# Optimization experiments

Measured on AMD Instinct MI355X. Metric: run time of the kernel, lower is better.

The kernel has to match this reference:

```python
import jax, jax.numpy as jnp
import numpy as np

jax.config.update("jax_enable_x64", True)

MAX_LEN = 2048
D_MODEL = 2048
CONTEXT = 1
FUDGE = 0.01
MIN_PERIOD = 1
MAX_PERIOD = 1024
FORGOTTEN_AT = 0.01


def _init_params():
    # Mirrors LaplaceAggregation.__init__ with init_method='linspace', modify_real=True
    limit = np.log(np.finfo(np.float64).max) / MAX_LEN - FUDGE
    soft_high = np.log(FORGOTTEN_AT) / MAX_PERIOD
    soft_low = np.log(FORGOTTEN_AT) / MIN_PERIOD
    a_low = max(-limit + FUDGE, soft_low)
    a_high = max(min(-1e-6, soft_high), a_low)
    a = np.linspace(a_low, a_high, D_MODEL).reshape(1, 1, D_MODEL, CONTEXT)
    b = (2.0 * np.pi / np.linspace(MIN_PERIOD, MAX_PERIOD, D_MODEL)).reshape(1, 1, D_MODEL, CONTEXT)
    return jnp.asarray(a, jnp.float64), jnp.asarray(b, jnp.float64)


def setup_inputs() -> dict:
    key = jax.random.key(0)
    k1, k2, k3 = jax.random.split(key, 3)
    B, T, F = 8, 1024, D_MODEL
    x = jax.random.normal(k1, (B, T, F), dtype=jnp.float32)
    mem_real = jax.random.normal(k2, (B, 1, F, CONTEXT), dtype=jnp.float32)
    mem_imag = jax.random.normal(k3, (B, 1, F, CONTEXT), dtype=jnp.float32)
    a, b = _init_params()
    return {"x": x, "mem_real": mem_real, "mem_imag": mem_imag, "a": a, "b": b}


def reference(x, mem_real, mem_imag, a, b):
    # batched_recurrent_update path (1 < T < max_len)
    T = x.shape[1]
    f64, c128 = jnp.float64, jnp.complex128
    ab = a.astype(f64) + 1j * b.astype(f64)           # [1,1,F,C] complex

    def psi(t):  # t: [T] -> [1,T,F,C]
        return jnp.exp(ab * t.reshape(1, -1, 1, 1))

    # inner_idx[:T] = [max_len-1, ..., max_len-T]; outer_idx = -inner_idx
    inner = jnp.arange(MAX_LEN - 1, MAX_LEN - 1 - T, -1, dtype=f64)
    offset = jnp.arange(1, T + 1, dtype=f64)          # state_offset[:T]

    xc = x.astype(f64)[..., None].astype(c128)        # [B,T,F,1]
    z = jnp.cumsum(psi(inner) * xc, axis=1)           # [B,T,F,C]
    mem0 = (mem_real.astype(f64) + 1j * mem_imag.astype(f64))  # [B,1,F,C]
    out = psi(-inner) * z + mem0 * psi(offset)        # [B,T,F,C]
    return out.astype(jnp.complex64)
```

## Files before the change

kernel.cpp:

```cpp
#include <hip/hip_runtime.h>
#include <math.h>

#define BB 8
#define TT 1024
#define FF 2048
#define F4 (FF / 4)
#define F2H (FF / 2)
#define LCH 16
#define NCH 64
#define THR 512


typedef float vf4 __attribute__((ext_vector_type(4)));

__device__ __align__(16) float g_S[(size_t)BB * NCH * FF * 2];
__device__ __align__(16) float g_seed[(size_t)BB * NCH * FF * 2];
__device__ __align__(16) float g_lam[FF * 2];

__device__ inline bool ab_is_f64(const void* bp) {
    double bd = ((const double*)bp)[0];
    return (bd > 6.0 && bd < 6.6);
}

__device__ inline void load_ab4(const void* ap, const void* bp, int f,
                                double* av, double* bv) {
    if (ab_is_f64(bp)) {
#pragma unroll
        for (int k = 0; k < 4; ++k) {
            av[k] = ((const double*)ap)[f + k];
            bv[k] = ((const double*)bp)[f + k];
        }
    } else {
#pragma unroll
        for (int k = 0; k < 4; ++k) {
            av[k] = (double)((const float*)ap)[f + k];
            bv[k] = (double)((const float*)bp)[f + k];
        }
    }
}

__global__ void __launch_bounds__(THR)
k_reduce(const float4* __restrict__ x4, const void* __restrict__ a,
         const void* __restrict__ b) {
    int tid = threadIdx.x;
    int c   = blockIdx.x & (NCH - 1);
    int bb  = blockIdx.x >> 6;

    const float4* xp = x4 + (size_t)(bb * TT + c * LCH) * F4 + tid;
    float4 xv[LCH];
#pragma unroll
    for (int j = 0; j < LCH; ++j) xv[j] = xp[(size_t)j * F4];

    double av[4], bv[4];
    load_ab4(a, b, 4 * tid, av, bv);
    float lr[4], li[4];
#pragma unroll
    for (int k = 0; k < 4; ++k) {
        double m = exp(av[k]);
        double s, cth;
        sincos(bv[k], &s, &cth);
        lr[k] = (float)(m * cth);
        li[k] = (float)(m * s);
    }
    if (blockIdx.x == 0) {
        vf4 t0, t1;
        t0.x = lr[0]; t0.y = li[0]; t0.z = lr[1]; t0.w = li[1];
        t1.x = lr[2]; t1.y = li[2]; t1.z = lr[3]; t1.w = li[3];
        *(vf4*)&g_lam[8 * tid]     = t0;
        *(vf4*)&g_lam[8 * tid + 4] = t1;
    }

    float zr[4] = {0.f, 0.f, 0.f, 0.f}, zi[4] = {0.f, 0.f, 0.f, 0.f};
#pragma unroll
    for (int j = 0; j < LCH; ++j) {
        float xj[4] = {xv[j].x, xv[j].y, xv[j].z, xv[j].w};
#pragma unroll
        for (int k = 0; k < 4; ++k) {
            float nr = fmaf(lr[k], zr[k], fmaf(-li[k], zi[k], xj[k]));
            float ni = fmaf(lr[k], zi[k], li[k] * zr[k]);
            zr[k] = nr; zi[k] = ni;
        }
    }
    float* sp = &g_S[((size_t)(bb * NCH + c) * FF + 4 * tid) * 2];
    vf4 s0, s1;
    s0.x = zr[0]; s0.y = zi[0]; s0.z = zr[1]; s0.w = zi[1];
    s1.x = zr[2]; s1.y = zi[2]; s1.z = zr[3]; s1.w = zi[3];
    *(vf4*)sp       = s0;
    *(vf4*)(sp + 4) = s1;
}

__global__ void __launch_bounds__(THR)
k_scan(const float* __restrict__ mr, const float* __restrict__ mi,
       const void* __restrict__ a, const void* __restrict__ b) {
    int gid = blockIdx.x * THR + threadIdx.x;
    int f   = gid & (FF - 1);
    int bb  = gid >> 11;

    double av, bvv;
    if (ab_is_f64(b)) {
        av  = ((const double*)a)[f];
        bvv = ((const double*)b)[f];
    } else {
        av  = (double)((const float*)a)[f];
        bvv = (double)((const float*)b)[f];
    }
    double mm = exp((double)LCH * av), ms, mc;
    sincos((double)LCH * bvv, &ms, &mc);
    double m_r = mm * mc, m_i = mm * ms;
    double m0r = (double)mr[(size_t)bb * FF + f];
    double m0i = (double)mi[(size_t)bb * FF + f];

    double e_r = 1.0, e_i = 0.0;
    double P_r = 0.0, P_i = 0.0;
    for (int cc = 0; cc < NCH; ++cc) {
        size_t idx = ((size_t)(bb * NCH + cc) * FF + f) * 2;
        g_seed[idx]     = (float)(e_r * m0r - e_i * m0i + P_r);
        g_seed[idx + 1] = (float)(e_r * m0i + e_i * m0r + P_i);
        double Sr = (double)g_S[idx], Si = (double)g_S[idx + 1];
        double npr = m_r * P_r - m_i * P_i + Sr;
        double npi = m_r * P_i + m_i * P_r + Si;
        P_r = npr; P_i = npi;
        double ner = e_r * m_r - e_i * m_i;
        double nei = e_r * m_i + e_i * m_r;
        e_r = ner; e_i = nei;
    }
}

__global__ void __launch_bounds__(THR)
k_final(const float4* __restrict__ x4, float2* __restrict__ out2, size_t limit2) {
    int tid = threadIdx.x;
    int c   = blockIdx.x & (NCH - 1);
    int bb  = blockIdx.x >> 6;

    const float4* xp = x4 + (size_t)(bb * TT + c * LCH) * F4 + tid;
    float4 xv[LCH];
#pragma unroll
    for (int j = 0; j < LCH; ++j) xv[j] = xp[(size_t)j * F4];

    const float4* lp = (const float4*)&g_lam[8 * tid];
    float4 lA = lp[0], lB = lp[1];
    float lr[4] = {lA.x, lA.z, lB.x, lB.z};
    float li[4] = {lA.y, lA.w, lB.y, lB.w};
    const float4* sp =
        (const float4*)&g_seed[((size_t)(bb * NCH + c) * FF + 4 * tid) * 2];
    float4 s0 = sp[0], s1 = sp[1];
    float wr[4] = {s0.x, s0.z, s1.x, s1.z};
    float wi[4] = {s0.y, s0.w, s1.y, s1.w};

    const size_t plane2 = (size_t)BB * TT * F2H;
    size_t row2 = (size_t)(bb * TT + c * LCH) * F2H + 2 * tid;
#pragma unroll
    for (int j = 0; j < LCH; ++j) {
        float xj[4] = {xv[j].x, xv[j].y, xv[j].z, xv[j].w};
#pragma unroll
        for (int k = 0; k < 4; ++k) {
            float nr = fmaf(lr[k], wr[k], fmaf(-li[k], wi[k], xj[k]));
            float ni = fmaf(lr[k], wi[k], li[k] * wr[k]);
            wr[k] = nr; wi[k] = ni;
        }
        size_t i2 = row2 + (size_t)j * F2H;
        if (i2 + 1 < limit2) {
            vf4 vr; vr.x = wr[0]; vr.y = wr[1]; vr.z = wr[2]; vr.w = wr[3];
            __builtin_nontemporal_store(vr, (vf4*)(out2 + i2));
        }
        size_t ii2 = i2 + plane2;
        if (ii2 + 1 < limit2) {
            vf4 vi; vi.x = wi[0]; vi.y = wi[1]; vi.z = wi[2]; vi.w = wi[3];
            __builtin_nontemporal_store(vi, (vf4*)(out2 + ii2));
        }
    }
}

extern "C" void kernel_launch(void* const* d_in, const int* in_sizes, int n_in,
                              void* d_out, int out_size, void* d_ws, size_t ws_size,
                              hipStream_t stream) {
    const float4* x4  = (const float4*)d_in[0];
    const float*  mr  = (const float*)d_in[1];
    const float*  mi  = (const float*)d_in[2];
    const void*   a   = d_in[3];
    const void*   b   = d_in[4];
    float2* out2 = (float2*)d_out;
    (void)d_ws; (void)ws_size; (void)n_in; (void)in_sizes;

    size_t limit2 = (size_t)out_size >> 1;

    k_reduce<<<BB * NCH, THR, 0, stream>>>(x4, a, b);
    k_scan<<<(BB * FF) / THR, THR, 0, stream>>>(mr, mi, a, b);
    k_final<<<BB * NCH, THR, 0, stream>>>(x4, out2, limit2);
}
```

Before: 143.6 us.

## Fuse chunk-carry scan into final kernel and double chunk length

Removes the separate sequential scan kernel: each final block now recomputes its own carry-in by combining all preceding chunk sums with lambda^32, and builds lambda^(32c) by repeated squaring in double. Chunk length doubles to 32 and chunk count halves, which shrinks the chunk-sum buffer and drops one launch plus the seed buffer round trip. In exchange every block re-reads up to 32 chunk sums and does redundant prefix work. The carry combine now runs in float instead of double, which may cost accuracy.

```diff
diff --git a/kernel.cpp b/kernel.cpp
--- a/kernel.cpp
+++ b/kernel.cpp
@@ -6,16 +6,15 @@
 #define FF 2048
 #define F4 (FF / 4)
 #define F2H (FF / 2)
-#define LCH 16
-#define NCH 64
+#define LCH 32
+#define NCH 32
 #define THR 512
 
 
 typedef float vf4 __attribute__((ext_vector_type(4)));
 
-__device__ __align__(16) float g_S[(size_t)BB * NCH * FF * 2];
-__device__ __align__(16) float g_seed[(size_t)BB * NCH * FF * 2];
-__device__ __align__(16) float g_lam[FF * 2];
+__device__ __align__(16) float  g_S[(size_t)BB * NCH * FF * 2];
+__device__ __align__(16) double g_lamd[FF * 2];
 
 __device__ inline bool ab_is_f64(const void* bp) {
     double bd = ((const double*)bp)[0];
@@ -44,36 +43,34 @@
          const void* __restrict__ b) {
     int tid = threadIdx.x;
     int c   = blockIdx.x & (NCH - 1);
-    int bb  = blockIdx.x >> 6;
-
-    const float4* xp = x4 + (size_t)(bb * TT + c * LCH) * F4 + tid;
-    float4 xv[LCH];
-#pragma unroll
-    for (int j = 0; j < LCH; ++j) xv[j] = xp[(size_t)j * F4];
+    int bb  = blockIdx.x >> 5;
 
     double av[4], bv[4];
     load_ab4(a, b, 4 * tid, av, bv);
-    float lr[4], li[4];
+    double lrd[4], lid[4];
 #pragma unroll
     for (int k = 0; k < 4; ++k) {
         double m = exp(av[k]);
-        double s, cth;
-        sincos(bv[k], &s, &cth);
-        lr[k] = (float)(m * cth);
-        li[k] = (float)(m * s);
+        double s, ct;
+        sincos(bv[k], &s, &ct);
+        lrd[k] = m * ct;
+        lid[k] = m * s;
     }
     if (blockIdx.x == 0) {
-        vf4 t0, t1;
-        t0.x = lr[0]; t0.y = li[0]; t0.z = lr[1]; t0.w = li[1];
-        t1.x = lr[2]; t1.y = li[2]; t1.z = lr[3]; t1.w = li[3];
-        *(vf4*)&g_lam[8 * tid]     = t0;
-        *(vf4*)&g_lam[8 * tid + 4] = t1;
-    }
-
+        double2* lt = (double2*)g_lamd + 4 * tid;
+#pragma unroll
+        for (int k = 0; k < 4; ++k) lt[k] = make_double2(lrd[k], lid[k]);
+    }
+    float lr[4], li[4];
+#pragma unroll
+    for (int k = 0; k < 4; ++k) { lr[k] = (float)lrd[k]; li[k] = (float)lid[k]; }
+
+    const float4* xp = x4 + (size_t)(bb * TT + c * LCH) * F4 + tid;
     float zr[4] = {0.f, 0.f, 0.f, 0.f}, zi[4] = {0.f, 0.f, 0.f, 0.f};
 #pragma unroll
     for (int j = 0; j < LCH; ++j) {
-        float xj[4] = {xv[j].x, xv[j].y, xv[j].z, xv[j].w};
+        float4 xv = xp[(size_t)j * F4];
+        float xj[4] = {xv.x, xv.y, xv.z, xv.w};
 #pragma unroll
         for (int k = 0; k < 4; ++k) {
             float nr = fmaf(lr[k], zr[k], fmaf(-li[k], zi[k], xj[k]));
@@ -81,91 +78,141 @@
             zr[k] = nr; zi[k] = ni;
         }
     }
-    float* sp = &g_S[((size_t)(bb * NCH + c) * FF + 4 * tid) * 2];
+    vf4* sp = (vf4*)&g_S[((size_t)(bb * NCH + c) * FF + 4 * tid) * 2];
     vf4 s0, s1;
     s0.x = zr[0]; s0.y = zi[0]; s0.z = zr[1]; s0.w = zi[1];
     s1.x = zr[2]; s1.y = zi[2]; s1.z = zr[3]; s1.w = zi[3];
-    *(vf4*)sp       = s0;
-    *(vf4*)(sp + 4) = s1;
+    sp[0] = s0;
+    sp[1] = s1;
 }
 
 __global__ void __launch_bounds__(THR)
-k_scan(const float* __restrict__ mr, const float* __restrict__ mi,
-       const void* __restrict__ a, const void* __restrict__ b) {
-    int gid = blockIdx.x * THR + threadIdx.x;
-    int f   = gid & (FF - 1);
-    int bb  = gid >> 11;
-
-    double av, bvv;
-    if (ab_is_f64(b)) {
-        av  = ((const double*)a)[f];
-        bvv = ((const double*)b)[f];
-    } else {
-        av  = (double)((const float*)a)[f];
-        bvv = (double)((const float*)b)[f];
-    }
-    double mm = exp((double)LCH * av), ms, mc;
-    sincos((double)LCH * bvv, &ms, &mc);
-    double m_r = mm * mc, m_i = mm * ms;
-    double m0r = (double)mr[(size_t)bb * FF + f];
-    double m0i = (double)mi[(size_t)bb * FF + f];
-
-    double e_r = 1.0, e_i = 0.0;
-    double P_r = 0.0, P_i = 0.0;
-    for (int cc = 0; cc < NCH; ++cc) {
-        size_t idx = ((size_t)(bb * NCH + cc) * FF + f) * 2;
-        g_seed[idx]     = (float)(e_r * m0r - e_i * m0i + P_r);
-        g_seed[idx + 1] = (float)(e_r * m0i + e_i * m0r + P_i);
-        double Sr = (double)g_S[idx], Si = (double)g_S[idx + 1];
-        double npr = m_r * P_r - m_i * P_i + Sr;
-        double npi = m_r * P_i + m_i * P_r + Si;
-        P_r = npr; P_i = npi;
-        double ner = e_r * m_r - e_i * m_i;
-        double nei = e_r * m_i + e_i * m_r;
-        e_r = ner; e_i = nei;
-    }
-}
-
-__global__ void __launch_bounds__(THR)
-k_final(const float4* __restrict__ x4, float2* __restrict__ out2, size_t limit2) {
+k_final(const float4* __restrict__ x4, const float* __restrict__ mr,
+        const float* __restrict__ mi, float2* __restrict__ out2, size_t limit2) {
     int tid = threadIdx.x;
     int c   = blockIdx.x & (NCH - 1);
-    int bb  = blockIdx.x >> 6;
+    int bb  = blockIdx.x >> 5;
+
+    float4 M0r = ((const float4*)mr)[(size_t)bb * F4 + tid];
+    float4 M0i = ((const float4*)mi)[(size_t)bb * F4 + tid];
+    float m0r[4] = {M0r.x, M0r.y, M0r.z, M0r.w};
+    float m0i[4] = {M0i.x, M0i.y, M0i.z, M0i.w};
+
+    const double2* lt = (const double2*)g_lamd + 4 * tid;
+    double lrd[4], lid[4];
+#pragma unroll
+    for (int k = 0; k < 4; ++k) { double2 d = lt[k]; lrd[k] = d.x; lid[k] = d.y; }
+
+    double mrd[4], mid[4];
+#pragma unroll
+    for (int k = 0; k < 4; ++k) { mrd[k] = lrd[k]; mid[k] = lid[k]; }
+#pragma unroll
+    for (int s = 0; s < 5; ++s)
+#pragma unroll
+        for (int k = 0; k < 4; ++k) {
+            double nr = mrd[k] * mrd[k] - mid[k] * mid[k];
+            double ni = 2.0 * mrd[k] * mid[k];
+            mrd[k] = nr; mid[k] = ni;
+        }
+    float m32r[4], m32i[4];
+#pragma unroll
+    for (int k = 0; k < 4; ++k) { m32r[k] = (float)mrd[k]; m32i[k] = (float)mid[k]; }
+
+    const vf4* Sp = (const vf4*)g_S + (size_t)bb * NCH * (FF / 2) + 2 * tid;
+    float Pr[4] = {0.f, 0.f, 0.f, 0.f}, Pi[4] = {0.f, 0.f, 0.f, 0.f};
+#pragma unroll
+    for (int blk = 0; blk < 4; ++blk) {
+        vf4 sA[8], sB[8];
+#pragma unroll
+        for (int u = 0; u < 8; ++u) {
+            int cc = blk * 8 + u;
+            sA[u] = Sp[(size_t)cc * (FF / 2)];
+            sB[u] = Sp[(size_t)cc * (FF / 2) + 1];
+        }
+#pragma unroll
+        for (int u = 0; u < 8; ++u) {
+            int cc = blk * 8 + u;
+            bool g = (cc < c);
+            float sr[4] = {sA[u].x, sA[u].z, sB[u].x, sB[u].z};
+            float si[4] = {sA[u].y, sA[u].w, sB[u].y, sB[u].w};
+#pragma unroll
+            for (int k = 0; k < 4; ++k) {
+                float gr = g ? m32r[k] : 1.f;
+                float gi = g ? m32i[k] : 0.f;
+                float gsr = g ? sr[k] : 0.f;
+                float gsi = g ? si[k] : 0.f;
+                float nr = fmaf(gr, Pr[k], fmaf(-gi, Pi[k], gsr));
+                float ni = fmaf(gr, Pi[k], fmaf(gi, Pr[k], gsi));
+                Pr[k] = nr; Pi[k] = ni;
+            }
+        }
+    }
+
+    double er[4] = {1.0, 1.0, 1.0, 1.0}, ei[4] = {0.0, 0.0, 0.0, 0.0};
+    {
+        double br_[4], bi_[4];
+#pragma unroll
+        for (int k = 0; k < 4; ++k) { br_[k] = lrd[k]; bi_[k] = lid[k]; }
+#pragma unroll
+        for (int s = 0; s < 5; ++s)
+#pragma unroll
+            for (int k = 0; k < 4; ++k) {
+                double nr = br_[k] * br_[k] - bi_[k] * bi_[k];
+                double ni = 2.0 * br_[k] * bi_[k];
+                br_[k] = nr; bi_[k] = ni;
+            }
+        int cbits = c;
+#pragma unroll
+        for (int bit = 0; bit < 5; ++bit) {
+            if (cbits & 1) {
+#pragma unroll
+                for (int k = 0; k < 4; ++k) {
+                    double nr = er[k] * br_[k] - ei[k] * bi_[k];
+                    double ni = er[k] * bi_[k] + ei[k] * br_[k];
+                    er[k] = nr; ei[k] = ni;
+                }
+            }
+            cbits >>= 1;
+#pragma unroll
+            for (int k = 0; k < 4; ++k) {
+                double nr = br_[k] * br_[k] - bi_[k] * bi_[k];
+                double ni = 2.0 * br_[k] * bi_[k];
+                br_[k] = nr; bi_[k] = ni;
+            }
+        }
+    }
+
+    float Wr[4], Wi[4];
+#pragma unroll
+    for (int k = 0; k < 4; ++k) {
+        Wr[k] = fmaf((float)er[k], m0r[k], fmaf(-(float)ei[k], m0i[k], Pr[k]));
+        Wi[k] = fmaf((float)er[k], m0i[k], fmaf((float)ei[k], m0r[k], Pi[k]));
+    }
+    float lr[4], li[4];
+#pragma unroll
+    for (int k = 0; k < 4; ++k) { lr[k] = (float)lrd[k]; li[k] = (float)lid[k]; }
 
     const float4* xp = x4 + (size_t)(bb * TT + c * LCH) * F4 + tid;
-    float4 xv[LCH];
-#pragma unroll
-    for (int j = 0; j < LCH; ++j) xv[j] = xp[(size_t)j * F4];
-
-    const float4* lp = (const float4*)&g_lam[8 * tid];
-    float4 lA = lp[0], lB = lp[1];
-    float lr[4] = {lA.x, lA.z, lB.x, lB.z};
-    float li[4] = {lA.y, lA.w, lB.y, lB.w};
-    const float4* sp =
-        (const float4*)&g_seed[((size_t)(bb * NCH + c) * FF + 4 * tid) * 2];
-    float4 s0 = sp[0], s1 = sp[1];
-    float wr[4] = {s0.x, s0.z, s1.x, s1.z};
-    float wi[4] = {s0.y, s0.w, s1.y, s1.w};
-
     const size_t plane2 = (size_t)BB * TT * F2H;
     size_t row2 = (size_t)(bb * TT + c * LCH) * F2H + 2 * tid;
 #pragma unroll
     for (int j = 0; j < LCH; ++j) {
-        float xj[4] = {xv[j].x, xv[j].y, xv[j].z, xv[j].w};
-#pragma unroll
-        for (int k = 0; k < 4; ++k) {
-            float nr = fmaf(lr[k], wr[k], fmaf(-li[k], wi[k], xj[k]));
-            float ni = fmaf(lr[k], wi[k], li[k] * wr[k]);
-            wr[k] = nr; wi[k] = ni;
+        float4 xv = xp[(size_t)j * F4];
+        float xj[4] = {xv.x, xv.y, xv.z, xv.w};
+#pragma unroll
+        for (int k = 0; k < 4; ++k) {
+            float nr = fmaf(lr[k], Wr[k], fmaf(-li[k], Wi[k], xj[k]));
+            float ni = fmaf(lr[k], Wi[k], li[k] * Wr[k]);
+            Wr[k] = nr; Wi[k] = ni;
         }
         size_t i2 = row2 + (size_t)j * F2H;
         if (i2 + 1 < limit2) {
-            vf4 vr; vr.x = wr[0]; vr.y = wr[1]; vr.z = wr[2]; vr.w = wr[3];
+            vf4 vr; vr.x = Wr[0]; vr.y = Wr[1]; vr.z = Wr[2]; vr.w = Wr[3];
             __builtin_nontemporal_store(vr, (vf4*)(out2 + i2));
         }
         size_t ii2 = i2 + plane2;
         if (ii2 + 1 < limit2) {
-            vf4 vi; vi.x = wi[0]; vi.y = wi[1]; vi.z = wi[2]; vi.w = wi[3];
+            vf4 vi; vi.x = Wi[0]; vi.y = Wi[1]; vi.z = Wi[2]; vi.w = Wi[3];
             __builtin_nontemporal_store(vi, (vf4*)(out2 + ii2));
         }
     }
@@ -185,6 +232,5 @@
     size_t limit2 = (size_t)out_size >> 1;
 
     k_reduce<<<BB * NCH, THR, 0, stream>>>(x4, a, b);
-    k_scan<<<(BB * FF) / THR, THR, 0, stream>>>(mr, mi, a, b);
-    k_final<<<BB * NCH, THR, 0, stream>>>(x4, out2, limit2);
-}
+    k_final<<<BB * NCH, THR, 0, stream>>>(x4, mr, mi, out2, limit2);
+}
```

Result: slower. 165.1 us (+15.0%).
